# Optimization experiments

Hardware: AMD Instinct MI355X
Metric: run time of the kernel (lower is better)

The kernel has to match this reference:

```python
import jax, jax.numpy as jnp
import numpy as np

EMBED_DIM = 384
NUM_HEADS = 6
EPS = 1e-5

def _conv_proj(x, w_dw, gamma, beta, mean, var, stride):
    # x: [B,H,W,C]; depthwise 3x3 conv (groups=C), pad 1, then BN (inference), then flatten HW.
    C = x.shape[-1]
    y = jax.lax.conv_general_dilated(
        x, w_dw, window_strides=(stride, stride), padding=[(1, 1), (1, 1)],
        dimension_numbers=("NHWC", "HWIO", "NHWC"), feature_group_count=C)
    y = (y - mean) * jax.lax.rsqrt(var + EPS) * gamma + beta
    B, H, W, Cc = y.shape
    return y.reshape(B, H * W, Cc)

def _heads(x):
    # [B, L, C] -> [B, nH, L, hd]
    B, L, C = x.shape
    hd = C // NUM_HEADS
    return x.reshape(B, L, NUM_HEADS, hd).transpose(0, 2, 1, 3)

def setup_inputs() -> dict:
    key = jax.random.key(0)
    ks = jax.random.split(key, 20)
    B, H, W, C = 64, 28, 28, EMBED_DIM
    inp = {
        "hidden_state": jax.random.normal(ks[0], (B, 1 + H * W, C), dtype=jnp.float32),
        "height": H,
        "width": W,
    }
    std = 0.02
    for i, p in enumerate(("q", "k", "v")):
        inp[f"w_dw_{p}"] = jax.random.normal(ks[1 + i], (3, 3, 1, C), dtype=jnp.float32) * std
        inp[f"bn_gamma_{p}"] = jnp.ones((C,), jnp.float32) + 0.1 * jax.random.normal(ks[4 + i], (C,))
        inp[f"bn_beta_{p}"] = 0.1 * jax.random.normal(ks[7 + i], (C,))
        inp[f"bn_mean_{p}"] = 0.1 * jax.random.normal(ks[10 + i], (C,))
        inp[f"bn_var_{p}"] = jnp.ones((C,), jnp.float32) + 0.1 * jax.random.uniform(ks[13 + i], (C,))
        inp[f"W_{p}"] = jax.random.normal(ks[16 + i], (C, C), dtype=jnp.float32) * std
        inp[f"b_{p}"] = jnp.zeros((C,), jnp.float32)
    return inp

def reference(hidden_state, height, width,
              w_dw_q, bn_gamma_q, bn_beta_q, bn_mean_q, bn_var_q, W_q, b_q,
              w_dw_k, bn_gamma_k, bn_beta_k, bn_mean_k, bn_var_k, W_k, b_k,
              w_dw_v, bn_gamma_v, bn_beta_v, bn_mean_v, bn_var_v, W_v, b_v):
    B, _, C = hidden_state.shape
    scale = C ** (-0.5)  # note: embed_dim**-0.5, as in the source
    cls_token = hidden_state[:, :1]
    x = hidden_state[:, 1:].reshape(B, height, width, C)

    q = _conv_proj(x, w_dw_q, bn_gamma_q, bn_beta_q, bn_mean_q, bn_var_q, stride=1)
    k = _conv_proj(x, w_dw_k, bn_gamma_k, bn_beta_k, bn_mean_k, bn_var_k, stride=2)
    v = _conv_proj(x, w_dw_v, bn_gamma_v, bn_beta_v, bn_mean_v, bn_var_v, stride=2)

    q = jnp.concatenate((cls_token, q), axis=1)
    k = jnp.concatenate((cls_token, k), axis=1)
    v = jnp.concatenate((cls_token, v), axis=1)

    q = _heads(q @ W_q + b_q)  # [B,h,Lq,d]
    k = _heads(k @ W_k + b_k)  # [B,h,Lk,d]
    v = _heads(v @ W_v + b_v)

    scores = jnp.einsum("bhqd,bhkd->bhqk", q, k) * scale
    probs = jax.nn.softmax(scores, axis=-1)
    ctx = jnp.einsum("bhqk,bhkd->bhqd", probs, v)
    Lq = ctx.shape[2]
    return ctx.transpose(0, 2, 1, 3).reshape(B, Lq, C)
```

## Files before the change

### kernel.cpp

```cpp
#include <hip/hip_runtime.h>
#include <hip/hip_bf16.h>

#define C_DIM 384
#define BATCH 64
#define LQ 785
#define LK 197
#define NHEADS 6
#define HDIM 64
#define QTILES 785
#define KTILES 197
#define KPAD 208

typedef __hip_bfloat16 bf16;
typedef __attribute__((ext_vector_type(8))) short short8;
typedef __attribute__((ext_vector_type(4))) float float4v;

__device__ __forceinline__ float bf2f(bf16 x) { return __bfloat162float(x); }
__device__ __forceinline__ bf16 f2bf(float x) { return __float2bfloat16(x); }
__device__ __forceinline__ float lo16f(unsigned int u) { return __uint_as_float(u << 16); }
__device__ __forceinline__ float hi16f(unsigned int u) { return __uint_as_float(u & 0xffff0000u); }
__device__ __forceinline__ unsigned short bfb(float x) {
    union { bf16 h; unsigned short s; } u; u.h = f2bf(x); return u.s;
}
__device__ __forceinline__ unsigned int pk2(float a, float b) {
    return ((unsigned int)bfb(b) << 16) | bfb(a);
}

template<bool F32>
__device__ __forceinline__ float ldx(const void* p, size_t i) {
    if constexpr (F32) return ((const float*)p)[i];
    else return bf2f(((const bf16*)p)[i]);
}
template<bool F32>
__device__ __forceinline__ void stx(void* p, size_t i, float v) {
    if constexpr (F32) ((float*)p)[i] = v;
    else ((bf16*)p)[i] = f2bf(v);
}
template<bool F32>
__device__ __forceinline__ void ld4(const void* p, size_t i, float* o) {
    if constexpr (F32) {
        float4 v = *(const float4*)((const float*)p + i);
        o[0] = v.x; o[1] = v.y; o[2] = v.z; o[3] = v.w;
    } else {
        uint2 u = *(const uint2*)((const bf16*)p + i);
        o[0] = lo16f(u.x); o[1] = hi16f(u.x); o[2] = lo16f(u.y); o[3] = hi16f(u.y);
    }
}
template<bool F32>
__device__ __forceinline__ void ld2(const void* p, size_t i, float* o) {
    if constexpr (F32) {
        float2 v = *(const float2*)((const float*)p + i);
        o[0] = v.x; o[1] = v.y;
    } else {
        unsigned int u = *(const unsigned int*)((const bf16*)p + i);
        o[0] = lo16f(u); o[1] = hi16f(u);
    }
}

__global__ void detect_kernel(const void* varq, int* flag) {
    const unsigned short* u = (const unsigned short*)varq;
    int votes = 0;
    #pragma unroll
    for (int i = 0; i < 4; ++i) {
        float b = __uint_as_float(((unsigned int)u[2 * i]) << 16);
        votes += (b > 0.5f && b < 2.0f) ? 1 : 0;
    }
    *flag = (votes == 4) ? 1 : 0;
}

template<bool F32>
__global__ __launch_bounds__(256) void repack_kernel(const int* __restrict__ flagp,
    const void* __restrict__ W0, const void* __restrict__ W1, const void* __restrict__ W2,
    bf16* __restrict__ dst)
{
    if (*flagp != (F32 ? 0 : 1)) return;
    const void* W = blockIdx.y == 0 ? W0 : (blockIdx.y == 1 ? W1 : W2);
    bf16* d = dst + (size_t)blockIdx.y * (C_DIM * C_DIM);
    int idx = blockIdx.x * 256 + threadIdx.x;
    int k = idx / C_DIM, nc = idx - k * C_DIM;
    int nt = nc >> 4, n = nc & 15, kt = k >> 5, q = (k >> 3) & 3, j = k & 7;
    d[(size_t)((((nt * 12 + kt) * 4 + q) * 16 + n) * 8 + j)] = f2bf(ldx<F32>(W, idx));
}

template<bool F32>
__device__ __forceinline__ void foldw(const void* __restrict__ wdw,
    const void* __restrict__ gamma, const void* __restrict__ beta,
    const void* __restrict__ mean,  const void* __restrict__ var,
    int c0, float w[9][2], float sh[2])
{
    float g[2], be[2], mu[2], vv[2];
    ld2<F32>(gamma, c0, g); ld2<F32>(beta, c0, be);
    ld2<F32>(mean,  c0, mu); ld2<F32>(var,  c0, vv);
    float sc[2];
    #pragma unroll
    for (int i = 0; i < 2; ++i) {
        sc[i] = g[i] * rsqrtf(vv[i] + 1e-5f);
        sh[i] = be[i] - mu[i] * sc[i];
    }
    #pragma unroll
    for (int p = 0; p < 9; ++p) {
        float t[2];
        ld2<F32>(wdw, (size_t)p * C_DIM + c0, t);
        w[p][0] = t[0] * sc[0];
        w[p][1] = t[1] * sc[1];
    }
}

template<int OJH, bool F32>
__device__ __forceinline__ void conv_quad(int b, int oik, int c2,
    const void* __restrict__ hs,
    const void* wq_, const void* gq, const void* beq, const void* muq, const void* vaq,
    const void* wk_, const void* gk, const void* bek, const void* muk, const void* vak,
    const void* wv_, const void* gv, const void* bev, const void* muv, const void* vav,
    bf16* __restrict__ qa, bf16* __restrict__ ka, bf16* __restrict__ va)
{
    int c0 = c2 * 2;
    float wq[9][2], wk[9][2], wv[9][2], shq[2], shk[2], shv[2];
    foldw<F32>(wq_, gq, beq, muq, vaq, c0, wq, shq);
    foldw<F32>(wk_, gk, bek, muk, vak, c0, wk, shk);
    foldw<F32>(wv_, gv, bev, muv, vav, c0, wv, shv);

    size_t hb = (size_t)b * (LQ * C_DIM);
    int i0 = 2 * oik - 1;
    bool rv[4];
    #pragma unroll
    for (int ri = 0; ri < 4; ++ri) rv[ri] = ((unsigned)(i0 + ri)) < 28u;

    float xw[4][3][2];
    constexpr int JJ0 = 14 * OJH - 1;

    int rq0 = b * LQ + 1 + 2 * oik * 28;
    int rq1 = rq0 + 28;
    int rk  = b * LK + 1 + oik * 14;

    #pragma unroll
    for (int s = 0; s < 16; ++s) {
        const int jj = JJ0 + s;
        const int sl = ((jj % 3) + 3) % 3;
        const bool cval = (jj >= 0) && (jj < 28);
        #pragma unroll
        for (int ri = 0; ri < 4; ++ri) {
            if (cval && rv[ri])
                ld2<F32>(hs, hb + (size_t)(1 + (i0 + ri) * 28 + jj) * C_DIM + c0, xw[ri][sl]);
            else { xw[ri][sl][0] = 0.f; xw[ri][sl][1] = 0.f; }
        }
        if (s >= 2) {
            const int jc = jj - 1;
            float a0[2] = {}, a1[2] = {};
            #pragma unroll
            for (int di = 0; di < 3; ++di)
                #pragma unroll
                for (int dj = 0; dj < 3; ++dj) {
                    const int s2 = (((jc - 1 + dj) % 3) + 3) % 3;
                    const int t = di * 3 + dj;
                    a0[0] = fmaf(xw[di][s2][0],     wq[t][0], a0[0]);
                    a0[1] = fmaf(xw[di][s2][1],     wq[t][1], a0[1]);
                    a1[0] = fmaf(xw[di + 1][s2][0], wq[t][0], a1[0]);
                    a1[1] = fmaf(xw[di + 1][s2][1], wq[t][1], a1[1]);
                }
            *(unsigned int*)&qa[(size_t)(rq0 + jc) * C_DIM + c0] = pk2(a0[0] + shq[0], a0[1] + shq[1]);
            *(unsigned int*)&qa[(size_t)(rq1 + jc) * C_DIM + c0] = pk2(a1[0] + shq[0], a1[1] + shq[1]);
            if ((jc & 1) == 0) {
                float k0[2] = {}, v0[2] = {};
                #pragma unroll
                for (int di = 0; di < 3; ++di)
                    #pragma unroll
                    for (int dj = 0; dj < 3; ++dj) {
                        const int s2 = (((jc - 1 + dj) % 3) + 3) % 3;
                        const int t = di * 3 + dj;
                        k0[0] = fmaf(xw[di][s2][0], wk[t][0], k0[0]);
                        k0[1] = fmaf(xw[di][s2][1], wk[t][1], k0[1]);
                        v0[0] = fmaf(xw[di][s2][0], wv[t][0], v0[0]);
                        v0[1] = fmaf(xw[di][s2][1], wv[t][1], v0[1]);
                    }
                int ro = rk + (jc >> 1);
                *(unsigned int*)&ka[(size_t)ro * C_DIM + c0] = pk2(k0[0] + shk[0], k0[1] + shk[1]);
                *(unsigned int*)&va[(size_t)ro * C_DIM + c0] = pk2(v0[0] + shv[0], v0[1] + shv[1]);
            }
        }
    }
}

#define CONV4_BLOCKS 960
template<bool F32>
__global__ __launch_bounds__(384) void conv4_kernel(
    const int* __restrict__ flagp, const void* __restrict__ hs,
    const void* wq, const void* gq, const void* beq, const void* muq, const void* vaq,
    const void* wk, const void* gk, const void* bek, const void* muk, const void* vak,
    const void* wv, const void* gv, const void* bev, const void* muv, const void* vav,
    bf16* __restrict__ qa, bf16* __restrict__ ka, bf16* __restrict__ va)
{
    if (*flagp != (F32 ? 0 : 1)) return;
    int bid = blockIdx.x;
    int tid = threadIdx.x;
    if (bid < 896) {
        int w = (bid & 7) * 112 + (bid >> 3);
        int b = w / 14, oik = w - b * 14;
        int c2 = tid % 192, ojh = tid / 192;
        if (ojh == 0)
            conv_quad<0, F32>(b, oik, c2, hs, wq, gq, beq, muq, vaq,
                              wk, gk, bek, muk, vak, wv, gv, bev, muv, vav, qa, ka, va);
        else
            conv_quad<1, F32>(b, oik, c2, hs, wq, gq, beq, muq, vaq,
                              wk, gk, bek, muk, vak, wv, gv, bev, muv, vav, qa, ka, va);
    } else {
        int b = bid - 896;
        if (tid < 192) {
            int c0 = tid * 2;
            float v2[2];
            ld2<F32>(hs, (size_t)b * (LQ * C_DIM) + c0, v2);
            unsigned int pk = pk2(v2[0], v2[1]);
            *(unsigned int*)&qa[(size_t)(b * LQ) * C_DIM + c0] = pk;
            *(unsigned int*)&ka[(size_t)(b * LK) * C_DIM + c0] = pk;
            *(unsigned int*)&va[(size_t)(b * LK) * C_DIM + c0] = pk;
        }
    }
}

__global__ __launch_bounds__(512) void gemm_lds_kernel(
    const int* __restrict__ flagp,
    const bf16* __restrict__ qa, const bf16* __restrict__ ka, const bf16* __restrict__ va,
    const bf16* __restrict__ wrep,
    const void* __restrict__ b_q, const void* __restrict__ b_k, const void* __restrict__ b_v,
    void* __restrict__ outq, bf16* __restrict__ kbuf, bf16* __restrict__ vbuf)
{
    __shared__ bf16 A_s[64 * C_DIM];

    const bool f32 = (*flagp == 0);
    int bidx = blockIdx.x;
    const bf16* A; const bf16* wr; const void* bias; int tile, mode;
    if (bidx < QTILES)                { mode = 0; tile = bidx;                  A = qa; wr = wrep;                          bias = b_q; }
    else if (bidx < QTILES + KTILES)  { mode = 1; tile = bidx - QTILES;         A = ka; wr = wrep + (size_t)C_DIM * C_DIM;     bias = b_k; }
    else                              { mode = 2; tile = bidx - QTILES - KTILES; A = va; wr = wrep + (size_t)2 * C_DIM * C_DIM; bias = b_v; }

    const bf16* Abase = A + (size_t)tile * (64 * C_DIM);
    int tid = threadIdx.x;
    int lane = tid & 63, wave = tid >> 6;
    int mrow = lane & 15, quad = lane >> 4;

    {
        int l4 = lane & 3, l16 = lane >> 2;
        #pragma unroll
        for (int i = 0; i < 6; ++i) {
            int t6 = wave * 6 + i;
            int rbase = (t6 / 3) * 4;
            int cbase = (t6 % 3) * 16;
            int row = rbase + l4;
            int ch  = cbase + l16;
            uint4 v = *(const uint4*)(Abase + (size_t)row * C_DIM + ch * 8);
            int dst = ch * 64 + (row ^ ((ch & 1) << 2));
            *(uint4*)&A_s[dst * 8] = v;
        }
    }
    __syncthreads();

    const short8* as = (const short8*)A_s;
    const short8* wf = (const short8*)wr;
    float4v acc[4][3] = {};

    #pragma unroll 2
    for (int kt = 0; kt < 12; ++kt) {
        short8 a[4];
        #pragma unroll
        for (int mt = 0; mt < 4; ++mt)
            a[mt] = as[(kt * 4 + quad) * 64 + ((mt * 16 + mrow) ^ ((quad & 1) << 2))];
        #pragma unroll
        for (int nt = 0; nt < 3; ++nt) {
            short8 bfrag = wf[(size_t)((wave * 3 + nt) * 12 + kt) * 64 + lane];
            #pragma unroll
            for (int mt = 0; mt < 4; ++mt)
                acc[mt][nt] = __builtin_amdgcn_mfma_f32_16x16x32_bf16(a[mt], bfrag, acc[mt][nt], 0, 0, 0);
        }
    }

    #pragma unroll
    for (int nt = 0; nt < 3; ++nt) {
        int col = wave * 48 + nt * 16 + mrow;
        float bb = f32 ? ((const float*)bias)[col] : bf2f(((const bf16*)bias)[col]);
        #pragma unroll
        for (int mt = 0; mt < 4; ++mt) {
            int row = tile * 64 + mt * 16 + quad * 4;
            #pragma unroll
            for (int r2 = 0; r2 < 4; ++r2) {
                float v = acc[mt][nt][r2] + bb;
                size_t o = (size_t)(row + r2) * C_DIM + col;
                if (mode == 0) {
                    if (f32) ((float*)outq)[o] = v;
                    else     ((bf16*)outq)[o] = f2bf(v);
                } else if (mode == 1) {
                    kbuf[o] = f2bf(v);
                } else {
                    vbuf[o] = f2bf(v);
                }
            }
        }
    }
}

__global__ __launch_bounds__(256) void vt_transpose_kernel(
    const bf16* __restrict__ v, bf16* __restrict__ vt)
{
    __shared__ unsigned short t[64][66];
    int bid = blockIdx.x;
    int ct = bid % 6; int tmp = bid / 6;
    int kt = tmp % 4; int b = tmp / 4;
    int k0 = kt * 64, c0 = ct * 64;
    int tid = threadIdx.x;

    for (int e = tid; e < 64 * 32; e += 256) {
        int r = e >> 5, c2 = e & 31;
        int k = k0 + r;
        unsigned int val = 0;
        if (k < LK) val = *(const unsigned int*)(v + ((size_t)b * LK + k) * C_DIM + c0 + c2 * 2);
        *(unsigned int*)&t[r][c2 * 2] = val;
    }
    __syncthreads();

    for (int e = tid; e < 64 * 32; e += 256) {
        int c = e >> 5, r2 = e & 31;
        int k = k0 + r2 * 2;
        if (k < KPAD) {
            unsigned int val = ((unsigned int)t[r2 * 2 + 1][c] << 16) | t[r2 * 2][c];
            *(unsigned int*)&vt[((size_t)(b * C_DIM + c0 + c)) * KPAD + k] = val;
        }
    }
}

template<int L, int OW, int STRIDE, bool F32, bool OF32>
__global__ __launch_bounds__(256) void fused_proj_kernel(
    const int* __restrict__ flagp,
    const void* __restrict__ hs, const void* __restrict__ wdw,
    const void* __restrict__ gamma, const void* __restrict__ beta,
    const void* __restrict__ mean,  const void* __restrict__ var,
    const bf16* __restrict__ Wrep,  const void* __restrict__ bias,
    void* __restrict__ O)
{
    if (*flagp != (F32 ? 0 : 1)) return;

    __shared__ bf16 A_s[64 * C_DIM];
    __shared__ float sc[C_DIM];
    __shared__ float sh[C_DIM];
    int tid = threadIdx.x;
    int m0 = blockIdx.x * 64;

    for (int c = tid; c < C_DIM; c += 256) {
        float s = ldx<F32>(gamma, c) * rsqrtf(ldx<F32>(var, c) + 1e-5f);
        sc[c] = s;
        sh[c] = ldx<F32>(beta, c) - ldx<F32>(mean, c) * s;
    }
    __syncthreads();

    for (int e = tid; e < 64 * 96; e += 256) {
        int m = e / 96;
        int c = (e - m * 96) * 4;
        int r = m0 + m;
        int b = r / L;
        int l = r - b * L;
        size_t hb = (size_t)b * (LQ * C_DIM);
        float v[4];
        if (l == 0) {
            ld4<F32>(hs, hb + c, v);
        } else {
            int p = l - 1;
            int oi = p / OW;
            int oj = p - oi * OW;
            float a0 = 0.f, a1 = 0.f, a2 = 0.f, a3 = 0.f;
            #pragma unroll
            for (int di = 0; di < 3; ++di) {
                int ii = oi * STRIDE - 1 + di;
                if (ii < 0 || ii >= 28) continue;
                #pragma unroll
                for (int dj = 0; dj < 3; ++dj) {
                    int jj = oj * STRIDE - 1 + dj;
                    if (jj < 0 || jj >= 28) continue;
                    float x[4], w[4];
                    ld4<F32>(hs, hb + (size_t)(1 + ii * 28 + jj) * C_DIM + c, x);
                    ld4<F32>(wdw, (size_t)(di * 3 + dj) * C_DIM + c, w);
                    a0 = fmaf(x[0], w[0], a0); a1 = fmaf(x[1], w[1], a1);
                    a2 = fmaf(x[2], w[2], a2); a3 = fmaf(x[3], w[3], a3);
                }
            }
            v[0] = a0 * sc[c + 0] + sh[c + 0];
            v[1] = a1 * sc[c + 1] + sh[c + 1];
            v[2] = a2 * sc[c + 2] + sh[c + 2];
            v[3] = a3 * sc[c + 3] + sh[c + 3];
        }
        int kt = c >> 5, q = (c >> 3) & 3, j = c & 7;
        int ofs = ((kt * 4 + q) * 64 + m) * 8 + j;
        ushort4 st = { bfb(v[0]), bfb(v[1]), bfb(v[2]), bfb(v[3]) };
        *(ushort4*)&A_s[ofs] = st;
    }
    __syncthreads();

    int lane = tid & 63, wave = tid >> 6;
    int mrow = lane & 15, quad = lane >> 4;
    float4v acc[4][6] = {};
    const short8* as = (const short8*)A_s;
    const short8* wr = (const short8*)Wrep;

    for (int kt = 0; kt < 12; ++kt) {
        short8 a[4];
        #pragma unroll
        for (int mt = 0; mt < 4; ++mt)
            a[mt] = as[(kt * 4 + quad) * 64 + mt * 16 + mrow];
        #pragma unroll
        for (int nt = 0; nt < 6; ++nt) {
            int ntg = wave * 6 + nt;
            short8 bfrag = wr[(size_t)(ntg * 12 + kt) * 64 + lane];
            #pragma unroll
            for (int mt = 0; mt < 4; ++mt)
                acc[mt][nt] = __builtin_amdgcn_mfma_f32_16x16x32_bf16(a[mt], bfrag, acc[mt][nt], 0, 0, 0);
        }
    }

    #pragma unroll
    for (int nt = 0; nt < 6; ++nt) {
        int col = wave * 96 + nt * 16 + mrow;
        float bb = ldx<F32>(bias, col);
        #pragma unroll
        for (int mt = 0; mt < 4; ++mt) {
            int row = m0 + mt * 16 + quad * 4;
            #pragma unroll
            for (int r2 = 0; r2 < 4; ++r2)
                stx<OF32>(O, (size_t)(row + r2) * C_DIM + col, acc[mt][nt][r2] + bb);
        }
    }
}

template<bool F32>
__global__ __launch_bounds__(256) void attn_vt_kernel(
    const int* __restrict__ flagp,
    const bf16* __restrict__ kg,
    const bf16* __restrict__ vt_g,
    void* __restrict__ qo)
{
    if (*flagp != (F32 ? 0 : 1)) return;

    __shared__ unsigned short Kf[8 * 2 * 64 * 8];
    __shared__ unsigned short Vt[64 * 128];
    __shared__ unsigned short Ps[4 * 16 * 128];

    int tid = threadIdx.x;
    int lane = tid & 63, wave = tid >> 6;
    int m = lane & 15, quad = lane >> 4;
    int bid = blockIdx.x;
    int qb = bid % 13;
    int bh = bid / 13;
    int h = bh % NHEADS, b = bh / NHEADS;
    int qbase = qb * 64 + wave * 16;

    int rev4m = ((m & 1) << 3) | ((m & 2) << 1) | ((m & 4) >> 1) | ((m & 8) >> 3);
    int revr[4];
    #pragma unroll
    for (int r = 0; r < 4; ++r) {
        int rr = quad * 4 + r;
        revr[r] = ((rr & 1) << 3) | ((rr & 2) << 1) | ((rr & 4) >> 1) | ((rr & 8) >> 3);
    }

    int qrow = min(qbase + m, LQ - 1);
    size_t qoff = ((size_t)b * LQ + qrow) * C_DIM + h * HDIM;
    short8 aq[2];
    #pragma unroll
    for (int ks = 0; ks < 2; ++ks) {
        float t[8];
        ld4<F32>(qo, qoff + ks * 32 + quad * 8, t);
        ld4<F32>(qo, qoff + ks * 32 + quad * 8 + 4, t + 4);
        short8 f;
        #pragma unroll
        for (int j = 0; j < 8; ++j) f[j] = (short)bfb(t[j]);
        aq[ks] = f;
    }

    const float scale = 0.05103103630798287f;
    float4v ctx[4] = {};
    float lsum4[4] = {};
    size_t kvbase = (size_t)b * LK * C_DIM + h * HDIM;
    size_t vtbase = (size_t)(b * C_DIM + h * HDIM) * KPAD;

    for (int c = 0; c < 2; ++c) {
        int c0 = c * 128;
        for (int e = tid; e < 1024; e += 256) {
            int col = e >> 3, d8 = e & 7;
            int gcol = c0 + col;
            uint4 val = {0, 0, 0, 0};
            if (gcol < LK) val = *(const uint4*)(kg + kvbase + (size_t)gcol * C_DIM + d8 * 8);
            int nt = col >> 4, n = col & 15, ks = d8 >> 2, q = d8 & 3;
            *(uint4*)&Kf[((nt * 2 + ks) * 64 + q * 16 + n) * 8] = val;
        }
        for (int e = tid; e < 1024; e += 256) {
            int d = e >> 4, kc = e & 15;
            uint4 val = {0, 0, 0, 0};
            if (c0 + kc * 8 < KPAD)
                val = *(const uint4*)(vt_g + vtbase + (size_t)d * KPAD + c0 + kc * 8);
            *(uint4*)&Vt[(d << 7) + ((kc ^ (d & 15)) << 3)] = val;
        }
        __syncthreads();

        const short8* kf = (const short8*)Kf;
        unsigned short* pw = Ps + wave * (16 * 128);
        int ntmax = (c == 0) ? 8 : 5;
        for (int nt = 0; nt < ntmax; ++nt) {
            float4v s = {0.f, 0.f, 0.f, 0.f};
            #pragma unroll
            for (int ks = 0; ks < 2; ++ks)
                s = __builtin_amdgcn_mfma_f32_16x16x32_bf16(aq[ks], kf[(nt * 2 + ks) * 64 + lane], s, 0, 0, 0);
            int coln = c0 + nt * 16 + m;
            bool valid = coln < LK;
            int chb = nt * 2 + (m >> 3);
            int sub = m & 7;
            #pragma unroll
            for (int r = 0; r < 4; ++r) {
                float pv = valid ? __expf(s[r] * scale) : 0.f;
                lsum4[r] += pv;
                pw[(((quad * 4 + r)) << 7) + ((chb ^ revr[r]) << 3) + sub] = bfb(pv);
            }
        }
        if (c == 1) {
            int sub = m & 7;
            #pragma unroll
            for (int nt = 5; nt < 8; ++nt) {
                int chb = nt * 2 + (m >> 3);
                #pragma unroll
                for (int r = 0; r < 4; ++r)
                    pw[(((quad * 4 + r)) << 7) + ((chb ^ revr[r]) << 3) + sub] = 0;
            }
        }

        const short8* vts = (const short8*)Vt;
        const short8* pf = (const short8*)Ps;
        #pragma unroll
        for (int ks = 0; ks < 4; ++ks) {
            short8 ap = pf[wave * 256 + (m << 4) + ((ks * 4 + quad) ^ rev4m)];
            #pragma unroll
            for (int ntv = 0; ntv < 4; ++ntv) {
                short8 bf_ = vts[((ntv * 16 + m) << 4) + ((ks * 4 + quad) ^ m)];
                ctx[ntv] = __builtin_amdgcn_mfma_f32_16x16x32_bf16(ap, bf_, ctx[ntv], 0, 0, 0);
            }
        }
        __syncthreads();
    }

    float inv[4];
    #pragma unroll
    for (int r = 0; r < 4; ++r) {
        float t = lsum4[r];
        t += __shfl_xor(t, 1);
        t += __shfl_xor(t, 2);
        t += __shfl_xor(t, 4);
        t += __shfl_xor(t, 8);
        inv[r] = 1.f / t;
    }
    #pragma unroll
    for (int ntv = 0; ntv < 4; ++ntv) {
        #pragma unroll
        for (int r = 0; r < 4; ++r) {
            int row = qbase + quad * 4 + r;
            if (row < LQ)
                stx<F32>(qo, ((size_t)b * LQ + row) * C_DIM + h * HDIM + ntv * 16 + m, ctx[ntv][r] * inv[r]);
        }
    }
}

template<bool F32>
__global__ __launch_bounds__(256) void attn_kernel(
    const int* __restrict__ flagp,
    const bf16* __restrict__ kg,
    const bf16* __restrict__ vg,
    void* __restrict__ qo)
{
    if (*flagp != (F32 ? 0 : 1)) return;

    __shared__ unsigned short Kf[8 * 2 * 64 * 8];
    __shared__ unsigned short Vf[4 * 4 * 64 * 8];
    __shared__ unsigned short Ps[4 * 16 * 136];

    int tid = threadIdx.x;
    int lane = tid & 63, wave = tid >> 6;
    int m = lane & 15, quad = lane >> 4;
    int bid = blockIdx.x;
    int qb = bid % 13;
    int bh = bid / 13;
    int h = bh % NHEADS, b = bh / NHEADS;
    int qbase = qb * 64 + wave * 16;

    int qrow = min(qbase + m, LQ - 1);
    size_t qoff = ((size_t)b * LQ + qrow) * C_DIM + h * HDIM;
    short8 aq[2];
    #pragma unroll
    for (int ks = 0; ks < 2; ++ks) {
        float t[8];
        ld4<F32>(qo, qoff + ks * 32 + quad * 8, t);
        ld4<F32>(qo, qoff + ks * 32 + quad * 8 + 4, t + 4);
        short8 f;
        #pragma unroll
        for (int j = 0; j < 8; ++j) f[j] = (short)bfb(t[j]);
        aq[ks] = f;
    }

    const float scale = 0.05103103630798287f;
    float4v ctx[4] = {};
    float lsum4[4] = {};
    size_t kvbase = (size_t)b * LK * C_DIM + h * HDIM;

    for (int c = 0; c < 2; ++c) {
        int c0 = c * 128;
        for (int e = tid; e < 1024; e += 256) {
            int col = e >> 3, d8 = e & 7;
            int gcol = c0 + col;
            uint4 val = {0, 0, 0, 0};
            if (gcol < LK) val = *(const uint4*)(kg + kvbase + (size_t)gcol * C_DIM + d8 * 8);
            int nt = col >> 4, n = col & 15, ks = d8 >> 2, q = d8 & 3;
            *(uint4*)&Kf[((nt * 2 + ks) * 64 + q * 16 + n) * 8] = val;
        }
        for (int e = tid; e < 1024; e += 256) {
            int p = e >> 3, d8 = e & 7;
            int gp = c0 + p;
            int ks = p >> 5, q = (p >> 3) & 3, j = p & 7;
            int ntv = d8 >> 1, nl0 = (d8 & 1) * 8;
            if (gp < LK) {
                union { uint4 u; unsigned short s[8]; } val;
                val.u = *(const uint4*)(vg + kvbase + (size_t)gp * C_DIM + d8 * 8);
                #pragma unroll
                for (int i = 0; i < 8; ++i)
                    Vf[((ntv * 4 + ks) * 64 + q * 16 + nl0 + i) * 8 + j] = val.s[i];
            } else {
                #pragma unroll
                for (int i = 0; i < 8; ++i)
                    Vf[((ntv * 4 + ks) * 64 + q * 16 + nl0 + i) * 8 + j] = 0;
            }
        }
        __syncthreads();

        const short8* kf = (const short8*)Kf;
        unsigned short* pw = Ps + wave * (16 * 136);
        int ntmax = (c == 0) ? 8 : 5;
        for (int nt = 0; nt < ntmax; ++nt) {
            float4v s = {0.f, 0.f, 0.f, 0.f};
            #pragma unroll
            for (int ks = 0; ks < 2; ++ks)
                s = __builtin_amdgcn_mfma_f32_16x16x32_bf16(aq[ks], kf[(nt * 2 + ks) * 64 + lane], s, 0, 0, 0);
            int coln = c0 + nt * 16 + m;
            bool valid = coln < LK;
            #pragma unroll
            for (int r = 0; r < 4; ++r) {
                float pv = valid ? __expf(s[r] * scale) : 0.f;
                lsum4[r] += pv;
                pw[(quad * 4 + r) * 136 + nt * 16 + m] = bfb(pv);
            }
        }
        if (c == 1) {
            #pragma unroll
            for (int nt = 5; nt < 8; ++nt)
                #pragma unroll
                for (int r = 0; r < 4; ++r)
                    pw[(quad * 4 + r) * 136 + nt * 16 + m] = 0;
        }

        const short8* vf = (const short8*)Vf;
        const short8* pf = (const short8*)Ps;
        #pragma unroll
        for (int ks = 0; ks < 4; ++ks) {
            short8 ap = pf[wave * 272 + m * 17 + ks * 4 + quad];
            #pragma unroll
            for (int ntv = 0; ntv < 4; ++ntv)
                ctx[ntv] = __builtin_amdgcn_mfma_f32_16x16x32_bf16(ap, vf[(ntv * 4 + ks) * 64 + lane], ctx[ntv], 0, 0, 0);
        }
        __syncthreads();
    }

    float inv[4];
    #pragma unroll
    for (int r = 0; r < 4; ++r) {
        float t = lsum4[r];
        t += __shfl_xor(t, 1);
        t += __shfl_xor(t, 2);
        t += __shfl_xor(t, 4);
        t += __shfl_xor(t, 8);
        inv[r] = 1.f / t;
    }
    #pragma unroll
    for (int ntv = 0; ntv < 4; ++ntv) {
        #pragma unroll
        for (int r = 0; r < 4; ++r) {
            int row = qbase + quad * 4 + r;
            if (row < LQ)
                stx<F32>(qo, ((size_t)b * LQ + row) * C_DIM + h * HDIM + ntv * 16 + m, ctx[ntv][r] * inv[r]);
        }
    }
}

extern "C" void kernel_launch(void* const* d_in, const int* in_sizes, int n_in,
                              void* d_out, int out_size, void* d_ws, size_t ws_size,
                              hipStream_t stream)
{
    const void* hs    = d_in[0];
    const void* wdw_q = d_in[3];
    const void* g_q   = d_in[4];
    const void* be_q  = d_in[5];
    const void* mu_q  = d_in[6];
    const void* va_q  = d_in[7];
    const void* W_q   = d_in[8];
    const void* b_q   = d_in[9];
    const void* wdw_k = d_in[10];
    const void* g_k   = d_in[11];
    const void* be_k  = d_in[12];
    const void* mu_k  = d_in[13];
    const void* va_k  = d_in[14];
    const void* W_k   = d_in[15];
    const void* b_k   = d_in[16];
    const void* wdw_v = d_in[17];
    const void* g_v   = d_in[18];
    const void* be_v  = d_in[19];
    const void* mu_v  = d_in[20];
    const void* va_v  = d_in[21];
    const void* W_v   = d_in[22];
    const void* b_v   = d_in[23];

    const size_t QA = (size_t)QTILES * 24576;
    const size_t KA = (size_t)KTILES * 24576;
    const size_t NEED_BIG = 16 + 2 * (3 * (size_t)C_DIM * C_DIM + QA + 4 * KA);

    int*  flag = (int*)d_ws;
    bf16* wrep = (bf16*)((char*)d_ws + 16);
    bf16* wrq  = wrep;
    bf16* wrk  = wrep + (size_t)C_DIM * C_DIM;
    bf16* wrv  = wrep + (size_t)2 * C_DIM * C_DIM;

    detect_kernel<<<1, 1, 0, stream>>>(va_q, flag);
    repack_kernel<false><<<dim3(576, 3), 256, 0, stream>>>(flag, W_q, W_k, W_v, wrep);
    repack_kernel<true ><<<dim3(576, 3), 256, 0, stream>>>(flag, W_q, W_k, W_v, wrep);

    if (ws_size >= NEED_BIG) {
        bf16* qa    = wrep + (size_t)3 * C_DIM * C_DIM;
        bf16* ka    = qa + QA;
        bf16* vaa   = ka + KA;
        bf16* kbuf  = vaa + KA;
        bf16* vbuf  = kbuf + KA;
        bf16* vbuft = qa;

        conv4_kernel<false><<<CONV4_BLOCKS, 384, 0, stream>>>(flag, hs,
            wdw_q, g_q, be_q, mu_q, va_q, wdw_k, g_k, be_k, mu_k, va_k,
            wdw_v, g_v, be_v, mu_v, va_v, qa, ka, vaa);
        conv4_kernel<true ><<<CONV4_BLOCKS, 384, 0, stream>>>(flag, hs,
            wdw_q, g_q, be_q, mu_q, va_q, wdw_k, g_k, be_k, mu_k, va_k,
            wdw_v, g_v, be_v, mu_v, va_v, qa, ka, vaa);

        gemm_lds_kernel<<<QTILES + 2 * KTILES, 512, 0, stream>>>(flag,
            qa, ka, vaa, wrep, b_q, b_k, b_v, d_out, kbuf, vbuf);

        vt_transpose_kernel<<<BATCH * 24, 256, 0, stream>>>(vbuf, vbuft);

        attn_vt_kernel<false><<<384 * 13, 256, 0, stream>>>(flag, kbuf, vbuft, d_out);
        attn_vt_kernel<true ><<<384 * 13, 256, 0, stream>>>(flag, kbuf, vbuft, d_out);
    } else {
        bf16* kbuf = wrep + (size_t)3 * C_DIM * C_DIM;
        bf16* vbuf = kbuf + (size_t)BATCH * LK * C_DIM;

        fused_proj_kernel<LQ, 28, 1, false, false><<<LQ, 256, 0, stream>>>(flag, hs, wdw_q, g_q, be_q, mu_q, va_q, wrq, b_q, d_out);
        fused_proj_kernel<LQ, 28, 1, true,  true ><<<LQ, 256, 0, stream>>>(flag, hs, wdw_q, g_q, be_q, mu_q, va_q, wrq, b_q, d_out);
        fused_proj_kernel<LK, 14, 2, false, false><<<LK, 256, 0, stream>>>(flag, hs, wdw_k, g_k, be_k, mu_k, va_k, wrk, b_k, kbuf);
        fused_proj_kernel<LK, 14, 2, true,  false><<<LK, 256, 0, stream>>>(flag, hs, wdw_k, g_k, be_k, mu_k, va_k, wrk, b_k, kbuf);
        fused_proj_kernel<LK, 14, 2, false, false><<<LK, 256, 0, stream>>>(flag, hs, wdw_v, g_v, be_v, mu_v, va_v, wrv, b_v, vbuf);
        fused_proj_kernel<LK, 14, 2, true,  false><<<LK, 256, 0, stream>>>(flag, hs, wdw_v, g_v, be_v, mu_v, va_v, wrv, b_v, vbuf);

        attn_kernel<false><<<384 * 13, 256, 0, stream>>>(flag, kbuf, vbuf, d_out);
        attn_kernel<true ><<<384 * 13, 256, 0, stream>>>(flag, kbuf, vbuf, d_out);
    }
}
```

Before: 355.2 us.

## Store Q as bf16 in place and transpose score MFMA for packed P writes

The Q projection now writes bf16 back into its own input buffer instead of writing fp32 or bf16 into the output, so attention loads Q fragments directly as bf16 vectors. The V-transpose buffer moves to the K input area to make room. The attention kernel swaps the MFMA operands to compute the transposed score tile, which lets each lane write probabilities as packed 64-bit LDS stores with an XOR swizzle and reduces the row-sum shuffle work. It also merges the two flag-templated launches into one kernel and remaps block indices so that each of the 8 XCDs works on contiguous batch-head groups for better cache locality. In exchange, Q is rounded to bf16 before attention in the fp32 path as well, and the gemm kernel overwrites its own input tiles in place.

```diff
diff --git a/kernel.cpp b/kernel.cpp
--- a/kernel.cpp
+++ b/kernel.cpp
@@ -219,10 +219,10 @@
 
 __global__ __launch_bounds__(512) void gemm_lds_kernel(
     const int* __restrict__ flagp,
-    const bf16* __restrict__ qa, const bf16* __restrict__ ka, const bf16* __restrict__ va,
+    bf16* __restrict__ qa, const bf16* __restrict__ ka, const bf16* __restrict__ va,
     const bf16* __restrict__ wrep,
     const void* __restrict__ b_q, const void* __restrict__ b_k, const void* __restrict__ b_v,
-    void* __restrict__ outq, bf16* __restrict__ kbuf, bf16* __restrict__ vbuf)
+    bf16* __restrict__ kbuf, bf16* __restrict__ vbuf)
 {
     __shared__ bf16 A_s[64 * C_DIM];
 
@@ -284,14 +284,9 @@
             for (int r2 = 0; r2 < 4; ++r2) {
                 float v = acc[mt][nt][r2] + bb;
                 size_t o = (size_t)(row + r2) * C_DIM + col;
-                if (mode == 0) {
-                    if (f32) ((float*)outq)[o] = v;
-                    else     ((bf16*)outq)[o] = f2bf(v);
-                } else if (mode == 1) {
-                    kbuf[o] = f2bf(v);
-                } else {
-                    vbuf[o] = f2bf(v);
-                }
+                if (mode == 0)      qa[o]   = f2bf(v);
+                else if (mode == 1) kbuf[o] = f2bf(v);
+                else                vbuf[o] = f2bf(v);
             }
         }
     }
@@ -427,53 +422,37 @@
     }
 }
 
-template<bool F32>
-__global__ __launch_bounds__(256) void attn_vt_kernel(
+__global__ __launch_bounds__(256) void attn_vt2_kernel(
     const int* __restrict__ flagp,
+    const bf16* __restrict__ qg,
     const bf16* __restrict__ kg,
     const bf16* __restrict__ vt_g,
-    void* __restrict__ qo)
-{
-    if (*flagp != (F32 ? 0 : 1)) return;
-
+    void* __restrict__ out)
+{
     __shared__ unsigned short Kf[8 * 2 * 64 * 8];
     __shared__ unsigned short Vt[64 * 128];
     __shared__ unsigned short Ps[4 * 16 * 128];
 
+    const bool f32 = (*flagp == 0);
     int tid = threadIdx.x;
     int lane = tid & 63, wave = tid >> 6;
     int m = lane & 15, quad = lane >> 4;
     int bid = blockIdx.x;
-    int qb = bid % 13;
-    int bh = bid / 13;
+    int w = (bid & 7) * 624 + (bid >> 3);
+    int qb = w % 13;
+    int bh = w / 13;
     int h = bh % NHEADS, b = bh / NHEADS;
     int qbase = qb * 64 + wave * 16;
 
-    int rev4m = ((m & 1) << 3) | ((m & 2) << 1) | ((m & 4) >> 1) | ((m & 8) >> 3);
-    int revr[4];
-    #pragma unroll
-    for (int r = 0; r < 4; ++r) {
-        int rr = quad * 4 + r;
-        revr[r] = ((rr & 1) << 3) | ((rr & 2) << 1) | ((rr & 4) >> 1) | ((rr & 8) >> 3);
-    }
-
     int qrow = min(qbase + m, LQ - 1);
-    size_t qoff = ((size_t)b * LQ + qrow) * C_DIM + h * HDIM;
-    short8 aq[2];
-    #pragma unroll
-    for (int ks = 0; ks < 2; ++ks) {
-        float t[8];
-        ld4<F32>(qo, qoff + ks * 32 + quad * 8, t);
-        ld4<F32>(qo, qoff + ks * 32 + quad * 8 + 4, t + 4);
-        short8 f;
-        #pragma unroll
-        for (int j = 0; j < 8; ++j) f[j] = (short)bfb(t[j]);
-        aq[ks] = f;
-    }
+    const bf16* qp = qg + ((size_t)b * LQ + qrow) * C_DIM + h * HDIM;
+    short8 bq[2];
+    bq[0] = *(const short8*)(qp + quad * 8);
+    bq[1] = *(const short8*)(qp + 32 + quad * 8);
 
     const float scale = 0.05103103630798287f;
     float4v ctx[4] = {};
-    float lsum4[4] = {};
+    float lsum = 0.f;
     size_t kvbase = (size_t)b * LK * C_DIM + h * HDIM;
     size_t vtbase = (size_t)(b * C_DIM + h * HDIM) * KPAD;
 
@@ -501,28 +480,25 @@
         int ntmax = (c == 0) ? 8 : 5;
         for (int nt = 0; nt < ntmax; ++nt) {
             float4v s = {0.f, 0.f, 0.f, 0.f};
-            #pragma unroll
-            for (int ks = 0; ks < 2; ++ks)
-                s = __builtin_amdgcn_mfma_f32_16x16x32_bf16(aq[ks], kf[(nt * 2 + ks) * 64 + lane], s, 0, 0, 0);
-            int coln = c0 + nt * 16 + m;
-            bool valid = coln < LK;
-            int chb = nt * 2 + (m >> 3);
-            int sub = m & 7;
+            s = __builtin_amdgcn_mfma_f32_16x16x32_bf16(kf[(nt * 2 + 0) * 64 + lane], bq[0], s, 0, 0, 0);
+            s = __builtin_amdgcn_mfma_f32_16x16x32_bf16(kf[(nt * 2 + 1) * 64 + lane], bq[1], s, 0, 0, 0);
+            int kb = c0 + nt * 16 + quad * 4;
+            float pv[4];
             #pragma unroll
             for (int r = 0; r < 4; ++r) {
-                float pv = valid ? __expf(s[r] * scale) : 0.f;
-                lsum4[r] += pv;
-                pw[(((quad * 4 + r)) << 7) + ((chb ^ revr[r]) << 3) + sub] = bfb(pv);
-            }
+                pv[r] = (kb + r < LK) ? __expf(s[r] * scale) : 0.f;
+                lsum += pv[r];
+            }
+            int chunk = (nt * 2 + (quad >> 1)) ^ m;
+            uint2 pk; pk.x = pk2(pv[0], pv[1]); pk.y = pk2(pv[2], pv[3]);
+            *(uint2*)&pw[m * 128 + chunk * 8 + (quad & 1) * 4] = pk;
         }
         if (c == 1) {
-            int sub = m & 7;
+            uint2 z = {0, 0};
             #pragma unroll
             for (int nt = 5; nt < 8; ++nt) {
-                int chb = nt * 2 + (m >> 3);
-                #pragma unroll
-                for (int r = 0; r < 4; ++r)
-                    pw[(((quad * 4 + r)) << 7) + ((chb ^ revr[r]) << 3) + sub] = 0;
+                int chunk = (nt * 2 + (quad >> 1)) ^ m;
+                *(uint2*)&pw[m * 128 + chunk * 8 + (quad & 1) * 4] = z;
             }
         }
 
@@ -530,7 +506,7 @@
         const short8* pf = (const short8*)Ps;
         #pragma unroll
         for (int ks = 0; ks < 4; ++ks) {
-            short8 ap = pf[wave * 256 + (m << 4) + ((ks * 4 + quad) ^ rev4m)];
+            short8 ap = pf[wave * 256 + m * 16 + ((ks * 4 + quad) ^ m)];
             #pragma unroll
             for (int ntv = 0; ntv < 4; ++ntv) {
                 short8 bf_ = vts[((ntv * 16 + m) << 4) + ((ks * 4 + quad) ^ m)];
@@ -540,23 +516,22 @@
         __syncthreads();
     }
 
-    float inv[4];
-    #pragma unroll
-    for (int r = 0; r < 4; ++r) {
-        float t = lsum4[r];
-        t += __shfl_xor(t, 1);
-        t += __shfl_xor(t, 2);
-        t += __shfl_xor(t, 4);
-        t += __shfl_xor(t, 8);
-        inv[r] = 1.f / t;
-    }
+    lsum += __shfl_xor(lsum, 16);
+    lsum += __shfl_xor(lsum, 32);
+    float inv = 1.f / lsum;
+
     #pragma unroll
     for (int ntv = 0; ntv < 4; ++ntv) {
         #pragma unroll
         for (int r = 0; r < 4; ++r) {
             int row = qbase + quad * 4 + r;
-            if (row < LQ)
-                stx<F32>(qo, ((size_t)b * LQ + row) * C_DIM + h * HDIM + ntv * 16 + m, ctx[ntv][r] * inv[r]);
+            float iv = __shfl(inv, quad * 4 + r);
+            if (row < LQ) {
+                size_t o = ((size_t)b * LQ + row) * C_DIM + h * HDIM + ntv * 16 + m;
+                float v = ctx[ntv][r] * iv;
+                if (f32) ((float*)out)[o] = v;
+                else     ((bf16*)out)[o] = f2bf(v);
+            }
         }
     }
 }
@@ -736,7 +711,7 @@
         bf16* vaa   = ka + KA;
         bf16* kbuf  = vaa + KA;
         bf16* vbuf  = kbuf + KA;
-        bf16* vbuft = qa;
+        bf16* vbuft = ka;
 
         conv4_kernel<false><<<CONV4_BLOCKS, 384, 0, stream>>>(flag, hs,
             wdw_q, g_q, be_q, mu_q, va_q, wdw_k, g_k, be_k, mu_k, va_k,
@@ -746,12 +721,11 @@
             wdw_v, g_v, be_v, mu_v, va_v, qa, ka, vaa);
 
         gemm_lds_kernel<<<QTILES + 2 * KTILES, 512, 0, stream>>>(flag,
-            qa, ka, vaa, wrep, b_q, b_k, b_v, d_out, kbuf, vbuf);
+            qa, ka, vaa, wrep, b_q, b_k, b_v, kbuf, vbuf);
 
         vt_transpose_kernel<<<BATCH * 24, 256, 0, stream>>>(vbuf, vbuft);
 
-        attn_vt_kernel<false><<<384 * 13, 256, 0, stream>>>(flag, kbuf, vbuft, d_out);
-        attn_vt_kernel<true ><<<384 * 13, 256, 0, stream>>>(flag, kbuf, vbuft, d_out);
+        attn_vt2_kernel<<<384 * 13, 256, 0, stream>>>(flag, qa, kbuf, vbuft, d_out);
     } else {
         bf16* kbuf = wrep + (size_t)3 * C_DIM * C_DIM;
         bf16* vbuf = kbuf + (size_t)BATCH * LK * C_DIM;
```

After: 333.5 us. -6.1%, faster.
